# Kernel optimization log

Hardware: AMD Instinct MI355X
Metric: run time of the kernel (lower is better)

Reference implementation:

```python
import jax, jax.numpy as jnp
import numpy as np
from jax import lax

PI = float(np.pi)
K_TOP = 128
N_BINS = 64

def _normalize(x, axis, eps=1e-12):
    n = jnp.sqrt(jnp.sum(x * x, axis=axis, keepdims=True))
    return x / jnp.maximum(n, eps)

def _conv(x, w, b):
    y = lax.conv_general_dilated(x, w, (1, 1), 'SAME',
                                 dimension_numbers=('NCHW', 'OIHW', 'NCHW'))
    return y + b[None, :, None, None]

def _maxpool2(x):
    return lax.reduce_window(x, -jnp.inf, lax.max, (1, 1, 2, 2), (1, 1, 2, 2), 'VALID')

def setup_inputs() -> dict:
    key = jax.random.key(0)
    ks = jax.random.split(key, 12)
    B, C, H, W = 16, 1, 512, 512
    PD, NPT = 128, 64
    fc_in = NPT + 64 * 4 * 4 + 3  # 1091
    def lin_init(k, fan_in, shape):
        bound = 1.0 / np.sqrt(fan_in)
        return jax.random.uniform(k, shape, jnp.float32, -bound, bound)
    return {
        'image': jax.random.normal(ks[0], (B, C, H, W), jnp.float32),
        'pattern_receptors': jax.random.normal(ks[1], (NPT, PD), jnp.float32) * 0.1,
        'conv1_w': lin_init(ks[2], 2 * 9, (32, 2, 3, 3)),
        'conv1_b': lin_init(ks[3], 2 * 9, (32,)),
        'conv2_w': lin_init(ks[4], 32 * 9, (64, 32, 3, 3)),
        'conv2_b': lin_init(ks[5], 32 * 9, (64,)),
        'fc1_w': lin_init(ks[6], fc_in, (512, fc_in)),
        'fc1_b': lin_init(ks[7], fc_in, (512,)),
        'fc2_w': lin_init(ks[8], 512, (PD, 512)),
        'fc2_b': lin_init(ks[9], 512, (PD,)),
        'ln_g': jnp.ones((PD,), jnp.float32),
        'ln_b': jnp.zeros((PD,), jnp.float32),
    }

def reference(image, pattern_receptors, conv1_w, conv1_b, conv2_w, conv2_b,
              fc1_w, fc1_b, fc2_w, fc2_b, ln_g, ln_b):
    B, C, H, W = image.shape
    # ---- frequency domain ----
    freq = jnp.fft.fft2(image, axes=(2, 3))
    magnitude = jnp.abs(freq)
    phase = jnp.angle(freq)
    # ---- pattern matching (topk of FFT magnitude vs receptor library) ----
    flat_mag = magnitude.reshape(B, C, -1)
    dom, _ = lax.top_k(flat_mag, K_TOP)          # [B, C, 128]
    dom = dom.reshape(B, -1)                     # [B, C*128]
    sims = jnp.matmul(_normalize(dom, 1), _normalize(pattern_receptors, 1).T)  # [B, 64]
    # ---- spatial path (original detaches via numpy roundtrip) ----
    img = lax.stop_gradient(image)
    gy = jnp.gradient(img, axis=2)
    gx = jnp.gradient(img, axis=3)
    gmag = jnp.sqrt(gx * gx + gy * gy)
    gori = jnp.arctan2(gy, gx)
    spat_in = jnp.stack([gmag, gori], axis=2).reshape(B, 2 * C, H, W)
    h = jax.nn.relu(_conv(spat_in, conv1_w, conv1_b))
    h = _maxpool2(h)                             # [B,32,H/2,W/2]
    h = jax.nn.relu(_conv(h, conv2_w, conv2_b))  # [B,64,H/2,W/2]
    Hp, Wp = h.shape[2], h.shape[3]
    h = h.reshape(B, 64, 4, Hp // 4, 4, Wp // 4).mean(axis=(3, 5))  # adaptive avg 4x4
    spatial = h.reshape(B, -1)                   # [B, 1024]
    # ---- phase statistics ----
    pf = phase.reshape(B, -1)
    p_mean = jnp.mean(pf, axis=1)
    p_std = jnp.std(pf, axis=1, ddof=1)
    bins = jnp.clip(jnp.floor((pf + PI) / (2 * PI) * N_BINS), 0, N_BINS - 1).astype(jnp.int32)
    hist = jnp.zeros((B, N_BINS), jnp.float32).at[jnp.arange(B)[:, None], bins].add(1.0)
    hist = hist / jnp.sum(hist, axis=1, keepdims=True)
    p_ent = -jnp.sum(hist * jnp.log(hist + 1e-10), axis=1)
    phase_feats = jnp.stack([p_mean, p_std, p_ent], axis=1)  # [B, 3]
    # ---- fuse: MLP + LayerNorm ----
    combined = jnp.concatenate([sims, spatial, phase_feats], axis=1)  # [B, 1091]
    z = jax.nn.relu(combined @ fc1_w.T + fc1_b)
    z = z @ fc2_w.T + fc2_b
    mu = jnp.mean(z, axis=-1, keepdims=True)
    var = jnp.var(z, axis=-1, keepdims=True)
    holo = (z - mu) / jnp.sqrt(var + 1e-5) * ln_g + ln_b
    return sims, spatial, phase_feats, holo
```

## Files before the change

### kernel.cpp

```cpp
#include <hip/hip_runtime.h>
#include <hip/hip_fp16.h>
#include <math.h>


#define PI_F 3.14159274f
#define TWO_PI_F 6.28318548f

typedef _Float16 half8 __attribute__((ext_vector_type(8)));
typedef _Float16 h2 __attribute__((ext_vector_type(2)));
typedef float floatx4 __attribute__((ext_vector_type(4)));

#define OFF_BIG   8388608
#define OFF_SMALL 25165824
#define NBIN 2048

__global__ void __launch_bounds__(256) init_kernel(float* __restrict__ zp,
                                                   float2* __restrict__ tw,
                                                   const float* __restrict__ w2,
                                                   const float* __restrict__ w1,
                                                   _Float16* __restrict__ wrep,
                                                   _Float16* __restrict__ w1r) {
    int idx = blockIdx.x * 256 + threadIdx.x;
    if (idx < 82992) zp[idx] = 0.0f;
    if (idx < 512) {
        if (idx == 0) tw[0] = make_float2(1.f, 0.f);
        else {
            int h = 31 - __clz(idx);
            int H = 1 << h;
            float sn, cs;
            sincosf(-PI_F * (float)(idx - H) / (float)H, &sn, &cs);
            tw[idx] = make_float2(cs, sn);
        }
    }
    if (idx < 18432) {
        int j = idx & 7;
        int lane = (idx >> 3) & 63;
        int nt = (idx >> 9) & 3;
        int tap = idx >> 11;
        int oc = nt * 16 + (lane & 15);
        int ic = (lane >> 4) * 8 + j;
        wrep[idx] = (_Float16)w2[(oc * 32 + ic) * 9 + tap];
    }
    if (idx < 1024) {
        int j = idx & 7;
        int lane = (idx >> 3) & 63;
        int nt = idx >> 9;
        int oc = 2 * (lane & 15) + nt;
        int k = (lane >> 4) * 8 + j;
        _Float16 v = (_Float16)0.f;
        if (k < 18) {
            int tap = k >> 1, ch = k & 1;
            v = (_Float16)w1[oc * 18 + ch * 9 + tap];
        }
        w1r[idx] = v;
    }
}

__global__ void __launch_bounds__(256) fft_rows2(const float* __restrict__ img,
                                                 const float2* __restrict__ twg,
                                                 h2* __restrict__ rowhf) {
    __shared__ float2 s[512];
    __shared__ float2 tw[512];
    const int t = threadIdx.x;
    const long long rbase = (long long)blockIdx.x * 1024;
    const float* x0 = img + rbase;
    const float* x1 = x0 + 512;

    for (int i = t; i < 512; i += 256) tw[i] = twg[i];
    for (int i = t; i < 512; i += 256) s[i] = make_float2(x0[i], x1[i]);
    __syncthreads();
#pragma unroll
    for (int st = 9; st >= 1; --st) {
        const int half = 1 << (st - 1);
        const int pos = t & (half - 1);
        const int grp = t >> (st - 1);
        const int i1 = (grp << st) + pos;
        const int i2 = i1 + half;
        float2 w = tw[half + pos];
        float2 a = s[i1], b = s[i2];
        float dx = a.x - b.x, dy = a.y - b.y;
        s[i1] = make_float2(a.x + b.x, a.y + b.y);
        s[i2] = make_float2(dx * w.x - dy * w.y, dx * w.y + dy * w.x);
        __syncthreads();
    }
    for (int i = t; i < 512; i += 256) {
        int k = __brev((unsigned)i) >> 23;
        int kp = (512 - k) & 511;
        int jp = __brev((unsigned)kp) >> 23;
        float2 Z = s[i], Zp = s[jp];
        rowhf[rbase + i]       = h2{(_Float16)(0.5f * (Z.x + Zp.x)),
                                    (_Float16)(0.5f * (Z.y - Zp.y))};
        rowhf[rbase + 512 + i] = h2{(_Float16)(0.5f * (Z.y + Zp.y)),
                                    (_Float16)(-0.5f * (Z.x - Zp.x))};
    }
}

#define FCOLS 16
__global__ void __launch_bounds__(512) fft_cols(const h2* __restrict__ rowhf,
                                                const float2* __restrict__ twg,
                                                _Float16* __restrict__ magT,
                                                float* __restrict__ psum,
                                                float* __restrict__ psumsq,
                                                unsigned* __restrict__ phist,
                                                unsigned* __restrict__ mhist) {
    __shared__ h2 sh[FCOLS * 512];
    __shared__ float2 tw[512];
    __shared__ unsigned ph[64];
    __shared__ unsigned mh[NBIN];
    __shared__ float red[16];
    const int t = threadIdx.x;
    const int b = blockIdx.x >> 5;
    const int x0 = (blockIdx.x & 31) * FCOLS;

    for (int i = t; i < 512; i += 512) tw[i] = twg[i];
    if (t < 64) ph[t] = 0u;
    for (int i = t; i < NBIN; i += 512) mh[i] = 0u;
    for (int idx = t; idx < FCOLS * 512; idx += 512) {
        int y = idx >> 4, c = idx & 15;
        sh[c * 512 + y] = rowhf[((size_t)(b * 512 + y)) * 512 + x0 + c];
    }
    __syncthreads();

    const int c = t >> 5;
    const int j = t & 31;
    float2 v[16];
#pragma unroll
    for (int r = 0; r < 16; ++r) {
        h2 hv = sh[c * 512 + j + 32 * r];
        v[r] = make_float2((float)hv[0], (float)hv[1]);
    }
#pragma unroll
    for (int r = 0; r < 8; ++r) {
        float2 w = tw[256 + j + 32 * r];
        float2 a = v[r], bb = v[r + 8];
        float dx = a.x - bb.x, dy = a.y - bb.y;
        v[r]     = make_float2(a.x + bb.x, a.y + bb.y);
        v[r + 8] = make_float2(dx * w.x - dy * w.y, dx * w.y + dy * w.x);
    }
#pragma unroll
    for (int g = 0; g < 2; ++g)
#pragma unroll
        for (int rr = 0; rr < 4; ++rr) {
            int r = g * 8 + rr;
            float2 w = tw[128 + j + 32 * rr];
            float2 a = v[r], bb = v[r + 4];
            float dx = a.x - bb.x, dy = a.y - bb.y;
            v[r]     = make_float2(a.x + bb.x, a.y + bb.y);
            v[r + 4] = make_float2(dx * w.x - dy * w.y, dx * w.y + dy * w.x);
        }
#pragma unroll
    for (int g = 0; g < 4; ++g)
#pragma unroll
        for (int rr = 0; rr < 2; ++rr) {
            int r = g * 4 + rr;
            float2 w = tw[64 + j + 32 * rr];
            float2 a = v[r], bb = v[r + 2];
            float dx = a.x - bb.x, dy = a.y - bb.y;
            v[r]     = make_float2(a.x + bb.x, a.y + bb.y);
            v[r + 2] = make_float2(dx * w.x - dy * w.y, dx * w.y + dy * w.x);
        }
    {
        float2 w = tw[32 + j];
#pragma unroll
        for (int g = 0; g < 8; ++g) {
            int r = g * 2;
            float2 a = v[r], bb = v[r + 1];
            float dx = a.x - bb.x, dy = a.y - bb.y;
            v[r]     = make_float2(a.x + bb.x, a.y + bb.y);
            v[r + 1] = make_float2(dx * w.x - dy * w.y, dx * w.y + dy * w.x);
        }
    }
#pragma unroll
    for (int hs = 4; hs >= 0; --hs) {
        const int h = 1 << hs;
        float2 w = tw[h + (j & (h - 1))];
        const bool upper = (j & h) != 0;
#pragma unroll
        for (int r = 0; r < 16; ++r) {
            float ox = __shfl_xor(v[r].x, h);
            float oy = __shfl_xor(v[r].y, h);
            float sx = v[r].x + ox, sy = v[r].y + oy;
            float dx = ox - v[r].x, dy = oy - v[r].y;
            float tx = dx * w.x - dy * w.y, ty = dx * w.y + dy * w.x;
            v[r].x = upper ? tx : sx;
            v[r].y = upper ? ty : sy;
        }
    }

    float lsum = 0.f, lsq = 0.f;
    _Float16* mcol = magT + ((size_t)(b * 512 + x0 + c)) * 512;
#pragma unroll
    for (int r = 0; r < 16; ++r) {
        float mag = sqrtf(v[r].x * v[r].x + v[r].y * v[r].y);
        union { _Float16 h; unsigned short u; } cvt;
        cvt.h = (_Float16)mag;
        mcol[j + 32 * r] = cvt.h;
        atomicAdd(&mh[min((unsigned)(cvt.u >> 4), (unsigned)(NBIN - 1))], 1u);
        float phv = atan2f(v[r].y, v[r].x);
        lsum += phv;
        lsq += phv * phv;
        int bin = min(max((int)floorf((phv + PI_F) / TWO_PI_F * 64.0f), 0), 63);
        atomicAdd(&ph[bin], 1u);
    }
    for (int off = 32; off > 0; off >>= 1) {
        lsum += __shfl_down(lsum, off);
        lsq  += __shfl_down(lsq, off);
    }
    if ((t & 63) == 0) { red[t >> 6] = lsum; red[8 + (t >> 6)] = lsq; }
    __syncthreads();
    if (t == 0) {
        float s = 0.f, q = 0.f;
        for (int i = 0; i < 8; ++i) { s += red[i]; q += red[8 + i]; }
        atomicAdd(psum + b, s);
        atomicAdd(psumsq + b, q);
    }
    if (t < 64 && ph[t]) atomicAdd(&phist[b * 64 + t], ph[t]);
    for (int i = t; i < NBIN; i += 512)
        if (mh[i]) atomicAdd(&mhist[b * NBIN + i], mh[i]);
}

__global__ void __launch_bounds__(256) thresh_kernel(const unsigned* __restrict__ mhist,
                                                     int* __restrict__ selbin) {
    __shared__ unsigned csum[256];
    const int b = blockIdx.x, t = threadIdx.x;
    unsigned s = 0;
    for (int i = 0; i < NBIN / 256; ++i) s += mhist[b * NBIN + t * (NBIN / 256) + i];
    csum[t] = s;
    __syncthreads();
    if (t == 0) {
        unsigned acc = 0; int chunk = 0;
        for (int i = 255; i >= 0; --i) {
            acc += csum[i];
            if (acc >= 128u) { chunk = i; break; }
        }
        unsigned acc2 = acc - csum[chunk];
        int tb = chunk * (NBIN / 256);
        for (int i = chunk * (NBIN / 256) + (NBIN / 256) - 1; i >= chunk * (NBIN / 256); --i) {
            acc2 += mhist[b * NBIN + i];
            if (acc2 >= 128u) { tb = i; break; }
        }
        selbin[b] = tb;
    }
}

#define TK_CAP 4096
__global__ void __launch_bounds__(256) collect_kernel(const _Float16* __restrict__ magT,
                                                      const int* __restrict__ selbin,
                                                      float* __restrict__ cand,
                                                      unsigned* __restrict__ ccnt) {
    const int blk = blockIdx.x;
    const int b = blk >> 4, chunk = blk & 15;
    const unsigned tb = (unsigned)selbin[b];
    const uint4* m = (const uint4*)(magT + (size_t)b * 262144 + chunk * 16384);
    float* cb = cand + b * TK_CAP;
    for (int i = threadIdx.x; i < 2048; i += 256) {
        uint4 v4 = m[i];
        unsigned vv[4] = {v4.x, v4.y, v4.z, v4.w};
#pragma unroll
        for (int j = 0; j < 4; ++j) {
#pragma unroll
            for (int k = 0; k < 2; ++k) {
                unsigned short ub = (k == 0) ? (unsigned short)(vv[j] & 0xFFFFu)
                                             : (unsigned short)(vv[j] >> 16);
                if ((unsigned)(ub >> 4) >= tb) {
                    unsigned p = atomicAdd(&ccnt[b], 1u);
                    if (p < TK_CAP) {
                        union { unsigned short u; _Float16 h; } c2;
                        c2.u = ub;
                        cb[p] = (float)c2.h;
                    }
                }
            }
        }
    }
}

__global__ void __launch_bounds__(1024) sort_kernel(const float* __restrict__ cand,
                                                    const unsigned* __restrict__ ccnt,
                                                    const float* __restrict__ rec,
                                                    float* __restrict__ comb,
                                                    float* __restrict__ dout) {
    __shared__ float c[TK_CAP];
    const int b = blockIdx.x, t = threadIdx.x;
    const unsigned n = min(ccnt[b], (unsigned)TK_CAP);
    int P = 256;
    while (P < (int)n) P <<= 1;
    for (int i = t; i < P; i += 1024) c[i] = (i < (int)n) ? cand[b * TK_CAP + i] : -1.0f;
    __syncthreads();
    for (int k = 2; k <= P; k <<= 1) {
        for (int j = k >> 1; j > 0; j >>= 1) {
            for (int i = t; i < P; i += 1024) {
                int ixj = i ^ j;
                if (ixj > i) {
                    float a = c[i], d = c[ixj];
                    bool up = ((i & k) == 0);
                    if (up ? (a < d) : (a > d)) { c[i] = d; c[ixj] = a; }
                }
            }
            __syncthreads();
        }
    }
    if (t < 64) {
        float dn = 0.f;
        for (int k = 0; k < 128; ++k) dn += c[k] * c[k];
        const float* rv = rec + t * 128;
        float rn = 0.f, dot = 0.f;
        for (int k = 0; k < 128; ++k) {
            float r = rv[k];
            rn += r * r;
            dot += c[k] * r;
        }
        float val = dot / (fmaxf(sqrtf(dn), 1e-12f) * fmaxf(sqrtf(rn), 1e-12f));
        dout[b * 64 + t] = val;
        comb[b * 1091 + t] = val;
    }
}

__global__ void __launch_bounds__(256) grad_conv1_mfma(const float* __restrict__ img,
                                                       const half8* __restrict__ w1r,
                                                       const float* __restrict__ c1b,
                                                       _Float16* __restrict__ h1) {
    __shared__ float simg[36 * 37];
    __shared__ _Float16 sgrad[(34 * 36 + 1) * 2];
    const int blk = blockIdx.x;
    const int b = blk >> 8;
    const int tr = blk & 255;
    const int TY = (tr >> 4) * 32, TX = (tr & 15) * 32;
    const int t = threadIdx.x;
    const float* im = img + (long long)b * 262144;

    for (int idx = t; idx < 1296; idx += 256) {
        int iy = idx / 36, ix = idx - iy * 36;
        int gy = min(max(TY - 2 + iy, 0), 511);
        int gx = min(max(TX - 2 + ix, 0), 511);
        simg[iy * 37 + ix] = im[gy * 512 + gx];
    }
    if (t == 0) { sgrad[2448] = (_Float16)0.f; sgrad[2449] = (_Float16)0.f; }
    __syncthreads();

    for (int idx = t; idx < 1156; idx += 256) {
        int ly = idx / 34, lx = idx - ly * 34;
        int gy = TY - 1 + ly, gx = TX - 1 + lx;
        float up = simg[ly * 37 + lx + 1];
        float dn = simg[(ly + 2) * 37 + lx + 1];
        float lf = simg[(ly + 1) * 37 + lx];
        float rt = simg[(ly + 1) * 37 + lx + 2];
        float fy = (gy <= 0 || gy >= 511) ? 1.f : 0.5f;
        float fx = (gx <= 0 || gx >= 511) ? 1.f : 0.5f;
        float gyv = (dn - up) * fy, gxv = (rt - lf) * fx;
        bool inside = ((unsigned)gy < 512u) && ((unsigned)gx < 512u);
        float mag = inside ? sqrtf(gxv * gxv + gyv * gyv) : 0.f;
        float ori = inside ? atan2f(gyv, gxv) : 0.f;
        int p = (ly * 36 + lx) * 2;
        sgrad[p] = (_Float16)mag;
        sgrad[p + 1] = (_Float16)ori;
    }
    __syncthreads();

    const int w = t >> 6, lane = t & 63;
    const int q = lane >> 4, m = lane & 15;
    const int oc0 = 2 * m;
    const float bias0 = c1b[oc0], bias1 = c1b[oc0 + 1];
    half8 Bf0 = w1r[lane], Bf1 = w1r[64 + lane];
    const unsigned* gp = (const unsigned*)sgrad;
    const int ZP = 1224;

    const int sy = (m >> 1) & 1, sx = m & 1, dqx = m >> 2;

#pragma unroll 4
    for (int i = 0; i < 16; ++i) {
        const int mt = w * 16 + i;
        const int qy = mt >> 2, qxg = mt & 3;
        const int py = 2 * qy + sy;
        const int px = 2 * (qxg * 4 + dqx) + sx;
        const int base = py * 36 + px;

        int o0 = (q == 0) ? base      : (q == 1) ? base + 37 : (q == 2) ? base + 74 : ZP;
        int o1 = (q == 0) ? base + 1  : (q == 1) ? base + 38 : ZP;
        int o2 = (q == 0) ? base + 2  : (q == 1) ? base + 72 : ZP;
        int o3 = (q == 0) ? base + 36 : (q == 1) ? base + 73 : ZP;

        union { unsigned u[4]; half8 h; } Af;
        Af.u[0] = gp[o0]; Af.u[1] = gp[o1]; Af.u[2] = gp[o2]; Af.u[3] = gp[o3];

        floatx4 acc0 = {bias0, bias0, bias0, bias0};
        floatx4 acc1 = {bias1, bias1, bias1, bias1};
        acc0 = __builtin_amdgcn_mfma_f32_16x16x32_f16(Af.h, Bf0, acc0, 0, 0, 0);
        acc1 = __builtin_amdgcn_mfma_f32_16x16x32_f16(Af.h, Bf1, acc1, 0, 0, 0);

        float v0 = fmaxf(fmaxf(acc0[0], acc0[1]), fmaxf(acc0[2], acc0[3]));
        float v1 = fmaxf(fmaxf(acc1[0], acc1[1]), fmaxf(acc1[2], acc1[3]));
        v0 = fmaxf(v0, 0.f);
        v1 = fmaxf(v1, 0.f);

        const int PY = (TY >> 1) + qy;
        const int PX = (TX >> 1) + qxg * 4 + q;
        _Float16* dst = h1 + (((size_t)(b * 256 + PY)) * 256 + PX) * 32;
        *(h2*)(dst + oc0) = h2{(_Float16)v0, (_Float16)v1};
    }
}

__global__ void __launch_bounds__(256) conv2_mfma(const _Float16* __restrict__ h1,
                                                  const _Float16* __restrict__ wrep,
                                                  const float* __restrict__ c2b,
                                                  float* __restrict__ sacc) {
    __shared__ _Float16 tile[18 * 34 * 32];
    __shared__ float lsum[64];
    const int blk = blockIdx.x;
    const int b  = blk >> 7;
    const int yt = (blk >> 3) & 15;
    const int xt = blk & 7;
    const int y0 = yt * 16, x0 = xt * 32;
    const int t = threadIdx.x;
    if (t < 64) lsum[t] = 0.f;

    for (int c = t; c < 18 * 136; c += 256) {
        int row = c / 136;
        int chunk = c - row * 136;
        int gy = y0 - 1 + row;
        int px = chunk >> 2;
        int gx = x0 - 1 + px;
        floatx4 v = {0.f, 0.f, 0.f, 0.f};
        if ((unsigned)gy < 256u && (unsigned)gx < 256u)
            v = *(const floatx4*)(h1 + (((size_t)(b * 256 + gy)) * 256 + gx) * 32 + (chunk & 3) * 8);
        *(floatx4*)(tile + (row * 34 + px) * 32 + (chunk & 3) * 8) = v;
    }
    __syncthreads();

    const int w = t >> 6, lane = t & 63;
    const int q = lane >> 4, ln15 = lane & 15;
    float bias[4];
#pragma unroll
    for (int nt = 0; nt < 4; ++nt) bias[nt] = c2b[nt * 16 + ln15];
    float partial[4] = {0.f, 0.f, 0.f, 0.f};

#pragma unroll 1
    for (int gr = 0; gr < 2; ++gr) {
        floatx4 acc[4][4];
#pragma unroll
        for (int mt = 0; mt < 4; ++mt)
#pragma unroll
            for (int nt = 0; nt < 4; ++nt)
                acc[mt][nt] = floatx4{bias[nt], bias[nt], bias[nt], bias[nt]};

        const _Float16* ab = tile + (((w * 4 + gr * 2) * 34) + ln15) * 32 + q * 8;
        const _Float16* wk = wrep + lane * 8;

#pragma unroll 1
        for (int ky = 0; ky < 3; ++ky) {
#pragma unroll
            for (int kx = 0; kx < 3; ++kx) {
                half8 Bf[4];
#pragma unroll
                for (int nt = 0; nt < 4; ++nt)
                    Bf[nt] = *(const half8*)(wk + (kx * 4 + nt) * 512);
#pragma unroll
                for (int mt = 0; mt < 4; ++mt) {
                    half8 Af = *(const half8*)(ab + (mt >> 1) * 1088 + (mt & 1) * 512 + kx * 32);
#pragma unroll
                    for (int nt = 0; nt < 4; ++nt)
                        acc[mt][nt] = __builtin_amdgcn_mfma_f32_16x16x32_f16(Af, Bf[nt], acc[mt][nt], 0, 0, 0);
                }
            }
            ab += 34 * 32;
            wk += 3 * 2048;
        }

#pragma unroll
        for (int mt = 0; mt < 4; ++mt)
#pragma unroll
            for (int nt = 0; nt < 4; ++nt)
#pragma unroll
                for (int rg = 0; rg < 4; ++rg)
                    partial[nt] += fmaxf(acc[mt][nt][rg], 0.f);
    }

#pragma unroll
    for (int nt = 0; nt < 4; ++nt) {
        float v = partial[nt];
        v += __shfl_xor(v, 16);
        v += __shfl_xor(v, 32);
        if (lane < 16) atomicAdd(&lsum[nt * 16 + ln15], v);
    }
    __syncthreads();
    const int cell = (yt >> 2) * 4 + (xt >> 1);
    if (t < 64) atomicAdd(&sacc[(((b << 6) + t) << 4) + cell], lsum[t]);
}

__global__ void __launch_bounds__(256) finalize_kernel(const float* __restrict__ sacc,
                                                       const float* __restrict__ psum,
                                                       const float* __restrict__ psumsq,
                                                       const unsigned* __restrict__ phist,
                                                       float* __restrict__ comb,
                                                       float* __restrict__ dout) {
    if (blockIdx.x < 64) {
        int idx = blockIdx.x * 256 + threadIdx.x;
        int b = idx >> 10, j = idx & 1023;
        float v = sacc[idx] * (1.0f / 4096.0f);
        dout[1024 + idx] = v;
        comb[b * 1091 + 64 + j] = v;
    } else {
        int t = threadIdx.x;
        if (t < 16) {
            const float N = 262144.f;
            float s = psum[t];
            float mean = s / N;
            float var = (psumsq[t] - s * s / N) / (N - 1.f);
            float sd = sqrtf(fmaxf(var, 0.f));
            float ent = 0.f;
            for (int i = 0; i < 64; ++i) {
                float p = (float)phist[t * 64 + i] / N;
                ent -= p * logf(p + 1e-10f);
            }
            dout[17408 + t * 3 + 0] = mean;
            dout[17408 + t * 3 + 1] = sd;
            dout[17408 + t * 3 + 2] = ent;
            float* cb = comb + t * 1091 + 1088;
            cb[0] = mean; cb[1] = sd; cb[2] = ent;
        }
    }
}

__global__ void __launch_bounds__(256) fc1_kernel(const float* __restrict__ comb,
                                                  const float* __restrict__ W1,
                                                  const float* __restrict__ B1,
                                                  float* __restrict__ out1) {
    const int wid = blockIdx.x * 4 + (threadIdx.x >> 6);
    const int lane = threadIdx.x & 63;
    const int b = wid >> 9, o = wid & 511;
    const float* w = W1 + (size_t)o * 1091;
    const float* c = comb + b * 1091;
    float acc = 0.f;
#pragma unroll 4
    for (int i = 0; i < 17; ++i) {
        int k = i * 64 + lane;
        acc += w[k] * c[k];
    }
    if (lane < 3) acc += w[1088 + lane] * c[1088 + lane];
#pragma unroll
    for (int off = 32; off > 0; off >>= 1) acc += __shfl_down(acc, off);
    if (lane == 0) out1[b * 512 + o] = fmaxf(acc + B1[o], 0.f);
}

__global__ void __launch_bounds__(256) fc2_kernel(const float* __restrict__ out1,
                                                  const float* __restrict__ W2,
                                                  const float* __restrict__ B2,
                                                  float* __restrict__ z) {
    const int wid = blockIdx.x * 4 + (threadIdx.x >> 6);
    const int lane = threadIdx.x & 63;
    const int b = wid >> 7, o = wid & 127;
    const float* w = W2 + (size_t)o * 512;
    const float* c = out1 + b * 512;
    float acc = 0.f;
#pragma unroll
    for (int i = 0; i < 8; ++i) {
        int k = i * 64 + lane;
        acc += w[k] * c[k];
    }
#pragma unroll
    for (int off = 32; off > 0; off >>= 1) acc += __shfl_down(acc, off);
    if (lane == 0) z[b * 128 + o] = acc + B2[o];
}

__global__ void __launch_bounds__(128) ln_kernel(const float* __restrict__ z,
                                                 const float* __restrict__ g,
                                                 const float* __restrict__ beta,
                                                 float* __restrict__ dout) {
    __shared__ float red[4];
    const int b = blockIdx.x, t = threadIdx.x;
    float acc = z[b * 128 + t];
    float s = acc;
    for (int off = 32; off > 0; off >>= 1) s += __shfl_down(s, off);
    if ((t & 63) == 0) red[t >> 6] = s;
    __syncthreads();
    float mu = (red[0] + red[1]) * (1.0f / 128.0f);
    float d = acc - mu;
    float q = d * d;
    for (int off = 32; off > 0; off >>= 1) q += __shfl_down(q, off);
    if ((t & 63) == 0) red[2 + (t >> 6)] = q;
    __syncthreads();
    float var = (red[2] + red[3]) * (1.0f / 128.0f);
    dout[17456 + b * 128 + t] = d / sqrtf(var + 1e-5f) * g[t] + beta[t];
}

extern "C" void kernel_launch(void* const* d_in, const int* in_sizes, int n_in,
                              void* d_out, int out_size, void* d_ws, size_t ws_size,
                              hipStream_t stream) {
    const float* img = (const float*)d_in[0];
    const float* rec = (const float*)d_in[1];
    const float* w1  = (const float*)d_in[2];
    const float* c1b = (const float*)d_in[3];
    const float* w2  = (const float*)d_in[4];
    const float* c2b = (const float*)d_in[5];
    const float* fw1 = (const float*)d_in[6];
    const float* fb1 = (const float*)d_in[7];
    const float* fw2 = (const float*)d_in[8];
    const float* fb2 = (const float*)d_in[9];
    const float* lng = (const float*)d_in[10];
    const float* lnb = (const float*)d_in[11];
    float* out = (float*)d_out;

    float* ws = (float*)d_ws;
    h2* rowhf       = (h2*)ws;
    _Float16* magT  = (_Float16*)(ws + OFF_BIG);
    _Float16* h1    = (_Float16*)(ws + OFF_BIG);
    float* small_  = ws + OFF_SMALL;
    float* sacc    = small_;
    float* psum    = small_ + 16384;
    float* psumsq  = small_ + 16400;
    unsigned* phist = (unsigned*)(small_ + 16416);
    unsigned* mhist = (unsigned*)(small_ + 17440);
    unsigned* ccnt  = (unsigned*)(small_ + 82976);
    int* selbin    = (int*)(small_ + 82992);
    float* comb    = small_ + 85056;
    float* out1    = small_ + 102512;
    _Float16* wrep = (_Float16*)(small_ + 110704);
    float2* twg    = (float2*)(small_ + 119920);
    float* cand    = small_ + 120944;
    float* zbuf    = cand;
    _Float16* w1r  = (_Float16*)(small_ + 186480);

    init_kernel<<<325, 256, 0, stream>>>(sacc, twg, w2, w1, wrep, w1r);
    fft_rows2<<<4096, 256, 0, stream>>>(img, twg, rowhf);
    fft_cols<<<512, 512, 0, stream>>>(rowhf, twg, magT, psum, psumsq, phist, mhist);
    thresh_kernel<<<16, 256, 0, stream>>>(mhist, selbin);
    collect_kernel<<<256, 256, 0, stream>>>(magT, selbin, cand, ccnt);
    sort_kernel<<<16, 1024, 0, stream>>>(cand, ccnt, rec, comb, out);
    grad_conv1_mfma<<<4096, 256, 0, stream>>>(img, (const half8*)w1r, c1b, h1);
    conv2_mfma<<<2048, 256, 0, stream>>>(h1, wrep, c2b, sacc);
    finalize_kernel<<<65, 256, 0, stream>>>(sacc, psum, psumsq, phist, comb, out);
    fc1_kernel<<<2048, 256, 0, stream>>>(comb, fw1, fb1, out1);
    fc2_kernel<<<512, 256, 0, stream>>>(out1, fw2, fb2, zbuf);
    ln_kernel<<<16, 128, 0, stream>>>(zbuf, lng, lnb, out);
}
```

Measured before the change: 272.4 us.

## Compute row FFTs per wavefront in registers using cross-lane shuffles

```diff
diff --git a/kernel.cpp b/kernel.cpp
--- a/kernel.cpp
+++ b/kernel.cpp
@@ -59,39 +59,98 @@
 __global__ void __launch_bounds__(256) fft_rows2(const float* __restrict__ img,
                                                  const float2* __restrict__ twg,
                                                  h2* __restrict__ rowhf) {
-    __shared__ float2 s[512];
+    __shared__ float2 sz[8 * 512];
     __shared__ float2 tw[512];
     const int t = threadIdx.x;
-    const long long rbase = (long long)blockIdx.x * 1024;
-    const float* x0 = img + rbase;
+    const int u = t >> 5;
+    const int j = t & 31;
+    const long long pair = (long long)blockIdx.x * 8 + u;
+    const float* x0 = img + pair * 1024;
     const float* x1 = x0 + 512;
 
     for (int i = t; i < 512; i += 256) tw[i] = twg[i];
-    for (int i = t; i < 512; i += 256) s[i] = make_float2(x0[i], x1[i]);
-    __syncthreads();
-#pragma unroll
-    for (int st = 9; st >= 1; --st) {
-        const int half = 1 << (st - 1);
-        const int pos = t & (half - 1);
-        const int grp = t >> (st - 1);
-        const int i1 = (grp << st) + pos;
-        const int i2 = i1 + half;
-        float2 w = tw[half + pos];
-        float2 a = s[i1], b = s[i2];
-        float dx = a.x - b.x, dy = a.y - b.y;
-        s[i1] = make_float2(a.x + b.x, a.y + b.y);
-        s[i2] = make_float2(dx * w.x - dy * w.y, dx * w.y + dy * w.x);
-        __syncthreads();
-    }
-    for (int i = t; i < 512; i += 256) {
+
+    float2 v[16];
+#pragma unroll
+    for (int r = 0; r < 16; ++r)
+        v[r] = make_float2(x0[j + 32 * r], x1[j + 32 * r]);
+    __syncthreads();
+
+#pragma unroll
+    for (int r = 0; r < 8; ++r) {
+        float2 w = tw[256 + j + 32 * r];
+        float2 a = v[r], bb = v[r + 8];
+        float dx = a.x - bb.x, dy = a.y - bb.y;
+        v[r]     = make_float2(a.x + bb.x, a.y + bb.y);
+        v[r + 8] = make_float2(dx * w.x - dy * w.y, dx * w.y + dy * w.x);
+    }
+#pragma unroll
+    for (int g = 0; g < 2; ++g)
+#pragma unroll
+        for (int rr = 0; rr < 4; ++rr) {
+            int r = g * 8 + rr;
+            float2 w = tw[128 + j + 32 * rr];
+            float2 a = v[r], bb = v[r + 4];
+            float dx = a.x - bb.x, dy = a.y - bb.y;
+            v[r]     = make_float2(a.x + bb.x, a.y + bb.y);
+            v[r + 4] = make_float2(dx * w.x - dy * w.y, dx * w.y + dy * w.x);
+        }
+#pragma unroll
+    for (int g = 0; g < 4; ++g)
+#pragma unroll
+        for (int rr = 0; rr < 2; ++rr) {
+            int r = g * 4 + rr;
+            float2 w = tw[64 + j + 32 * rr];
+            float2 a = v[r], bb = v[r + 2];
+            float dx = a.x - bb.x, dy = a.y - bb.y;
+            v[r]     = make_float2(a.x + bb.x, a.y + bb.y);
+            v[r + 2] = make_float2(dx * w.x - dy * w.y, dx * w.y + dy * w.x);
+        }
+    {
+        float2 w = tw[32 + j];
+#pragma unroll
+        for (int g = 0; g < 8; ++g) {
+            int r = g * 2;
+            float2 a = v[r], bb = v[r + 1];
+            float dx = a.x - bb.x, dy = a.y - bb.y;
+            v[r]     = make_float2(a.x + bb.x, a.y + bb.y);
+            v[r + 1] = make_float2(dx * w.x - dy * w.y, dx * w.y + dy * w.x);
+        }
+    }
+#pragma unroll
+    for (int hs = 4; hs >= 0; --hs) {
+        const int h = 1 << hs;
+        float2 w = tw[h + (j & (h - 1))];
+        const bool upper = (j & h) != 0;
+#pragma unroll
+        for (int r = 0; r < 16; ++r) {
+            float ox = __shfl_xor(v[r].x, h);
+            float oy = __shfl_xor(v[r].y, h);
+            float sx = v[r].x + ox, sy = v[r].y + oy;
+            float dx = ox - v[r].x, dy = oy - v[r].y;
+            float tx = dx * w.x - dy * w.y, ty = dx * w.y + dy * w.x;
+            v[r].x = upper ? tx : sx;
+            v[r].y = upper ? ty : sy;
+        }
+    }
+
+    float2* Z = sz + u * 512;
+#pragma unroll
+    for (int r = 0; r < 16; ++r) Z[j + 32 * r] = v[r];
+    __syncthreads();
+
+    h2* out0 = rowhf + pair * 1024;
+#pragma unroll
+    for (int r = 0; r < 16; ++r) {
+        int i = j + 32 * r;
         int k = __brev((unsigned)i) >> 23;
         int kp = (512 - k) & 511;
         int jp = __brev((unsigned)kp) >> 23;
-        float2 Z = s[i], Zp = s[jp];
-        rowhf[rbase + i]       = h2{(_Float16)(0.5f * (Z.x + Zp.x)),
-                                    (_Float16)(0.5f * (Z.y - Zp.y))};
-        rowhf[rbase + 512 + i] = h2{(_Float16)(0.5f * (Z.y + Zp.y)),
-                                    (_Float16)(-0.5f * (Z.x - Zp.x))};
+        float2 Zi = v[r], Zp = Z[jp];
+        out0[i]       = h2{(_Float16)(0.5f * (Zi.x + Zp.x)),
+                           (_Float16)(0.5f * (Zi.y - Zp.y))};
+        out0[512 + i] = h2{(_Float16)(0.5f * (Zi.y + Zp.y)),
+                           (_Float16)(-0.5f * (Zi.x - Zp.x))};
     }
 }
 
@@ -621,7 +680,7 @@
     _Float16* w1r  = (_Float16*)(small_ + 186480);
 
     init_kernel<<<325, 256, 0, stream>>>(sacc, twg, w2, w1, wrep, w1r);
-    fft_rows2<<<4096, 256, 0, stream>>>(img, twg, rowhf);
+    fft_rows2<<<512, 256, 0, stream>>>(img, twg, rowhf);
     fft_cols<<<512, 512, 0, stream>>>(rowhf, twg, magT, psum, psumsq, phist, mhist);
     thresh_kernel<<<16, 256, 0, stream>>>(mhist, selbin);
     collect_kernel<<<256, 256, 0, stream>>>(magT, selbin, cand, ccnt);
```

New measurement: 268.1 us. No clear change (-1.6%).
